# Kernel tuning notes

Hardware: AMD Instinct MI355X
Metric: run time of the kernel (lower is better)

## Reference

```python
import jax, jax.numpy as jnp
import numpy as np

NPG = 39      # nodes per graph, from (1+8+64+9)*(39+1)=3280 = lin1 in_features
NEG_SLOPE = 0.2


def gat_conv(x, src, dst, W, a_src, a_dst, b, n):
    """PyG GATConv, heads=1, self-loops already appended to (src, dst).
    x:[N,Fin] W:[Fin,Fout] a_src/a_dst:[Fout] b:[Fout] -> [N,Fout]"""
    h = x @ W                                        # [N,Fout]
    e = jax.nn.leaky_relu(h[src] @ a_src + h[dst] @ a_dst, NEG_SLOPE)  # [E]
    m = jax.lax.stop_gradient(jax.ops.segment_max(e, dst, num_segments=n))
    w = jnp.exp(e - m[dst])
    denom = jax.ops.segment_sum(w, dst, num_segments=n)
    alpha = w / (denom[dst] + 1e-16)                 # segment softmax per target node
    out = jax.ops.segment_sum(alpha[:, None] * h[src], dst, num_segments=n)
    return out + b


def setup_inputs() -> dict:
    key = jax.random.key(0)
    ks = jax.random.split(key, 20)
    B, DEG = 4096, 8
    N = B * NPG
    E = N * DEG
    x = jax.random.normal(ks[0], (N, 1), dtype=jnp.float32)
    # block-diagonal edges: each node emits DEG edges to random nodes in SAME graph
    src = jnp.repeat(jnp.arange(N, dtype=jnp.int64), DEG)
    offs = (src // NPG) * NPG
    dst = offs + jax.random.randint(ks[1], (E,), 0, NPG, dtype=jnp.int64)
    edge_index = jnp.stack([src, dst])
    batch_vec = jnp.repeat(jnp.arange(B, dtype=jnp.int64), NPG)

    def glorot(k, shape):
        fan = shape[0] + (shape[1] if len(shape) > 1 else 1)
        s = jnp.sqrt(6.0 / fan)
        return jax.random.uniform(k, shape, jnp.float32, -s, s)

    p = {
        'W1': glorot(ks[2], (1, 8)),   'a1s': glorot(ks[3], (8,)),  'a1d': glorot(ks[4], (8,)),  'b1': jnp.zeros((8,), jnp.float32),
        'W2': glorot(ks[5], (8, 64)),  'a2s': glorot(ks[6], (64,)), 'a2d': glorot(ks[7], (64,)), 'b2': jnp.zeros((64,), jnp.float32),
        'W3': glorot(ks[8], (64, 9)),  'a3s': glorot(ks[9], (9,)),  'a3d': glorot(ks[10], (9,)), 'b3': jnp.zeros((9,), jnp.float32),
        'lW1': glorot(ks[11], (3280, 5000)), 'lb1': jnp.zeros((5000,), jnp.float32),
        'lW2': glorot(ks[12], (5000, 1024)), 'lb2': jnp.zeros((1024,), jnp.float32),
        'lW3': glorot(ks[13], (1024, 9)),    'lb3': jnp.zeros((9,), jnp.float32),
    }
    return {'x': x, 'edge_index': edge_index, 'batch_vec': batch_vec, **p}


def reference(x, edge_index, batch_vec,
              W1, a1s, a1d, b1, W2, a2s, a2d, b2, W3, a3s, a3d, b3,
              lW1, lb1, lW2, lb2, lW3, lb3):
    N = x.shape[0]
    B = N // NPG
    loops = jnp.arange(N, dtype=edge_index.dtype)
    src = jnp.concatenate([edge_index[0], loops])   # GATConv add_self_loops=True
    dst = jnp.concatenate([edge_index[1], loops])

    res = x.reshape(B, -1)                                    # [B,39]
    out0 = jax.ops.segment_max(x, batch_vec, num_segments=B)  # [B,1]

    h1 = jax.nn.relu(gat_conv(x, src, dst, W1, a1s, a1d, b1, N))   # dropout = eval no-op
    res1 = h1.reshape(B, -1)                                   # [B,312]
    out1 = jax.ops.segment_max(h1, batch_vec, num_segments=B)

    h2 = jax.nn.relu(gat_conv(h1, src, dst, W2, a2s, a2d, b2, N))
    res2 = h2.reshape(B, -1)                                   # [B,2496]
    out2 = jax.ops.segment_max(h2, batch_vec, num_segments=B)

    h3 = jax.nn.relu(gat_conv(h2, src, dst, W3, a3s, a3d, b3, N))
    res3 = h3.reshape(B, -1)                                   # [B,351]
    out3 = jax.ops.segment_max(h3, batch_vec, num_segments=B)

    f = jnp.concatenate([res, res1, res2, res3, out0, out1, out2, out3], axis=1)  # [B,3280]
    f = jax.nn.relu(f @ lW1 + lb1)
    f = jax.nn.relu(f @ lW2 + lb2)
    return f @ lW3 + lb3                                       # [B,9]
```

## Files before the change

kernel.cpp:

```cpp
#include <hip/hip_runtime.h>
#include <hip/hip_bf16.h>
#include <hip/hip_fp16.h>
#include <stdint.h>


typedef float f32x4 __attribute__((ext_vector_type(4)));
typedef short bf16x8 __attribute__((ext_vector_type(8)));
typedef _Float16 f16x8 __attribute__((ext_vector_type(8)));

__device__ __forceinline__ unsigned fenc(float f) {
  int s = __float_as_int(f);
  return s < 0 ? ~(unsigned)s : ((unsigned)s | 0x80000000u);
}
__device__ __forceinline__ float fdec(unsigned u) {
  return (u & 0x80000000u) ? __int_as_float((int)(u & 0x7fffffffu))
                           : __int_as_float(~(int)u);
}

__device__ __forceinline__ void ldsbar() {
  asm volatile("s_waitcnt lgkmcnt(0)\n\ts_barrier" ::: "memory");
}


__global__ __launch_bounds__(128) void gnn_conv_seq(
    const float* __restrict__ x,
    const int* __restrict__ esrc, const int* __restrict__ edst,
    const float* __restrict__ W1, const float* __restrict__ a1s, const float* __restrict__ a1d, const float* __restrict__ b1,
    const float* __restrict__ W2, const float* __restrict__ a2s, const float* __restrict__ a2d, const float* __restrict__ b2,
    const float* __restrict__ W3, const float* __restrict__ a3s, const float* __restrict__ a3d, const float* __restrict__ b3,
    __hip_bfloat16* __restrict__ fA,
    const float* __restrict__ lW1, const float* __restrict__ lW2,
    short* __restrict__ W1T, short* __restrict__ W2T)
{
  __shared__ __align__(16) char smem[19200];
  const int tid = threadIdx.x;
  const int bid = blockIdx.x;

  if (bid >= 4096) {
    float (*t)[260] = (float(*)[260])smem;
    const int cid = bid - 4096;
    const float* W; short* WT; int ktile, ntile, K0, N0, KT;
    if (cid < 4160) { W = lW1; WT = W1T; ktile = cid % 208; ntile = cid / 208; K0 = 3280; N0 = 5000; KT = 52; }
    else { int c2 = cid - 4160; W = lW2; WT = W2T; ktile = c2 % 320; ntile = c2 / 320; K0 = 5000; N0 = 1024; KT = 80; }

    const int kb = ktile * 16, nb = ntile * 256;
    const int wv = tid >> 6, ln = tid & 63;
#pragma unroll
    for (int r = 0; r < 8; ++r) {
      int k = kb + wv * 8 + r;
      int n = nb + ln * 4;
      f32x4 v = (f32x4){0.f, 0.f, 0.f, 0.f};
      if (k < K0 && n < N0) v = *(const f32x4*)&W[(size_t)k * N0 + n];
      *(f32x4*)&t[wv * 8 + r][ln * 4] = v;
    }
    __syncthreads();
#pragma unroll
    for (int h = 0; h < 4; ++h) {
      int c = h * 128 + tid;
      int nl = c >> 1, kc = c & 1;
      int n = nb + nl, k = kb + kc * 8;
      union { bf16x8 v; __hip_bfloat16 b[8]; } z;
#pragma unroll
      for (int j = 0; j < 8; ++j) z.b[j] = __float2bfloat16(t[kc * 8 + j][nl]);
      int rt = n >> 7, mi = (n >> 4) & 7, lr = n & 15;
      int kt = k >> 6, kq = (k >> 5) & 1, lc = (k >> 3) & 3;
      size_t addr = ((((size_t)rt * KT) + kt) * 16 + mi * 2 + kq) * 512 + ((size_t)lr + 16 * lc) * 8;
      *(bf16x8*)&WT[addr] = z.v;
    }
    return;
  }

  float*    A     = (float*)   (smem);
  __half*   Hh2   = (__half*)  (smem + 6880);
  __half*   h1h   = (__half*)  (smem + 12512);
  float*    HfT   = (float*)   (smem + 13152);
  float*    sW3T  = (float*)   (smem + 14752);
  float*    xbuf  = (float*)   (smem + 17216);
  float*    a2buf = (float*)   (smem + 17376);
  float*    sarr  = (float*)   (smem + 17888);
  float*    darr  = (float*)   (smem + 18048);
  float*    den   = (float*)   (smem + 18208);
  unsigned* umax  = (unsigned*)(smem + 18368);
  unsigned* umx   = (unsigned*)(smem + 18528);
  float*    a3sb  = (float*)   (smem + 19056);
  float*    a3db  = (float*)   (smem + 19104);
  float*    b3b   = (float*)   (smem + 19152);

  const int g = bid, w = tid >> 6, f = tid & 63;

  const int rt = g >> 7, mi = (g >> 4) & 7, lrow = g & 15;
  const size_t gbase = (size_t)rt * 52 * 8192 + (size_t)(mi * 2) * 512 + (size_t)lrow * 8;
#define COLADDR(c) (gbase + (size_t)((c) >> 6) * 8192 + (size_t)(((c) >> 5) & 1) * 512 \
                    + (size_t)(((c) >> 3) & 3) * 128 + ((c) & 7))

  for (int i = tid; i < 576; i += 128) { int k = i / 9, f3 = i - 9 * k; sW3T[f3 * 68 + k] = W3[i]; }
  a2buf[tid] = (tid < 64) ? a2s[tid] : a2d[tid - 64];
  if (tid < 9) { a3sb[tid] = a3s[tid]; a3db[tid] = a3d[tid]; b3b[tid] = b3[tid]; }
  for (int i = tid; i < 132; i += 128) umx[i] = 0u;
  for (int i = tid; i < 430; i += 128) *(f32x4*)&A[i * 4] = (f32x4){0.f, 0.f, 0.f, 0.f};
  for (int i = tid; i < 400; i += 128) HfT[i] = 0.f;
  if (tid < 40) { den[tid] = 0.f; umax[tid] = 0u; xbuf[tid] = 0.f; }

  float xv = 0.f;
  if (tid < 39) { xv = x[g * 39 + tid]; xbuf[tid] = xv; fA[COLADDR(tid)] = __float2bfloat16(xv); }

  int els[3], eld[3];
  const int eb = g * 312, nb0 = g * 39;
#pragma unroll
  for (int it = 0; it < 3; ++it) {
    int e = it * 128 + tid, ls = -1, ld = 0;
    if (e < 351) {
      if (e < 312) { ls = esrc[eb + e] - nb0; ld = edst[eb + e] - nb0; }
      else         { ls = e - 312; ld = ls; }
    }
    els[it] = ls; eld[it] = ld;
  }
  float c_s = 0.f, c_d = 0.f;
  const float w1r = W1[tid & 7], b1r = b1[tid & 7];
#pragma unroll
  for (int ff = 0; ff < 8; ++ff) { float wv = W1[ff]; c_s += wv * a1s[ff]; c_d += wv * a1d[ff]; }
  ldsbar();

  if (tid < 39) atomicMax(&umx[0], fenc(xv));
  float ee[3];
#pragma unroll
  for (int it = 0; it < 3; ++it) {
    if (els[it] >= 0) {
      float e = xbuf[els[it]] * c_s + xbuf[eld[it]] * c_d;
      e = (e > 0.f) ? e : 0.2f * e;
      ee[it] = e;
      atomicMax(&umax[eld[it]], fenc(e));
    }
  }
  ldsbar();
#pragma unroll
  for (int it = 0; it < 3; ++it) {
    if (els[it] >= 0) {
      float wv = __expf(ee[it] - fdec(umax[eld[it]]));
      atomicAdd(&den[eld[it]], wv);
      atomicAdd(&A[eld[it] * 44 + els[it]], wv);
    }
  }
  ldsbar();
  if (tid < 39) {
    const float* Ar = &A[tid * 44];
    float q = 0.f;
#pragma unroll
    for (int c = 0; c < 10; ++c) {
      f32x4 a4 = *(const f32x4*)&Ar[c * 4];
      f32x4 x4 = *(const f32x4*)&xbuf[c * 4];
      q += a4.x * x4.x + a4.y * x4.y + a4.z * x4.z + a4.w * x4.w;
    }
    sarr[tid] = q * (1.f / (den[tid] + 1e-16f));
  }
  ldsbar();
#pragma unroll
  for (int it = 0; it < 3; ++it) {
    int slot = it * 128 + tid;
    if (slot < 312) {
      int i = slot >> 3, fi = slot & 7;
      float v = fmaxf(sarr[i] * w1r + b1r, 0.f);
      h1h[slot] = __float2half(v);
      fA[COLADDR(39 + slot)] = __float2bfloat16(v);
      atomicMax(&umx[1 + fi], fenc(v));
    }
  }
  ldsbar();

  float ht2r[40];
  {
    float w2k[8];
#pragma unroll
    for (int k = 0; k < 8; ++k) w2k[k] = W2[k * 64 + f];
#pragma unroll
    for (int i = 0; i < 39; ++i) {
      f16x8 hr = *(const f16x8*)&h1h[i * 8];
      float hv = 0.f;
#pragma unroll
      for (int k = 0; k < 8; ++k) hv += (float)hr[k] * w2k[k];
      ht2r[i] = hv;
    }
    ht2r[39] = 0.f;
#pragma unroll
    for (int i = 0; i < 39; ++i) {
      if ((i < 20) ? (w == 0) : (w == 1))
        Hh2[i * 72 + f] = __float2half(ht2r[i]);
    }
    for (int i = tid; i < 430; i += 128) *(f32x4*)&A[i * 4] = (f32x4){0.f, 0.f, 0.f, 0.f};
    if (tid < 39) { den[tid] = 0.f; umax[tid] = 0u; }
  }
  ldsbar();
  {
    int node = f;
    if (node < 39) {
      const float* ab = a2buf + (tid & 64);
      const __half* hr = &Hh2[node * 72];
      float s = 0.f;
#pragma unroll
      for (int c = 0; c < 8; ++c) {
        f16x8 hv = *(const f16x8*)&hr[c * 8];
        f32x4 a0 = *(const f32x4*)&ab[c * 8];
        f32x4 a1 = *(const f32x4*)&ab[c * 8 + 4];
        s += (float)hv[0] * a0.x + (float)hv[1] * a0.y + (float)hv[2] * a0.z + (float)hv[3] * a0.w
           + (float)hv[4] * a1.x + (float)hv[5] * a1.y + (float)hv[6] * a1.z + (float)hv[7] * a1.w;
      }
      if (tid < 64) sarr[node] = s; else darr[node] = s;
    }
  }
  ldsbar();
#pragma unroll
  for (int it = 0; it < 3; ++it) {
    if (els[it] >= 0) {
      float e = sarr[els[it]] + darr[eld[it]];
      e = (e > 0.f) ? e : 0.2f * e;
      ee[it] = e;
      atomicMax(&umax[eld[it]], fenc(e));
    }
  }
  ldsbar();
#pragma unroll
  for (int it = 0; it < 3; ++it) {
    if (els[it] >= 0) {
      float wv = __expf(ee[it] - fdec(umax[eld[it]]));
      atomicAdd(&den[eld[it]], wv);
      atomicAdd(&A[eld[it] * 44 + els[it]], wv);
    }
  }
  ldsbar();
  {
    const float b2r = b2[f];
    for (int it = 0; it < 20; ++it) {
      int i = it * 2 + w;
      if (i < 39) {
        float inv = 1.f / (den[i] + 1e-16f);
        const float* Ar = &A[i * 44];
        float acc = 0.f;
#pragma unroll
        for (int c = 0; c < 10; ++c) {
          f32x4 a4 = *(const f32x4*)&Ar[c * 4];
          acc += a4.x * ht2r[c * 4] + a4.y * ht2r[c * 4 + 1]
               + a4.z * ht2r[c * 4 + 2] + a4.w * ht2r[c * 4 + 3];
        }
        float v = fmaxf(acc * inv + b2r, 0.f);
        Hh2[i * 72 + f] = __float2half(v);
        fA[COLADDR(351 + i * 64 + f)] = __float2bfloat16(v);
        atomicMax(&umx[9 + f], fenc(v));
      }
    }
  }
  ldsbar();

  {
#pragma unroll
    for (int it = 0; it < 3; ++it) {
      int slot = it * 128 + tid;
      if (slot < 351) {
        int i = slot / 9, f3 = slot - 9 * i;
        const __half* hr = &Hh2[i * 72];
        const float* wr = &sW3T[f3 * 68];
        float acc = 0.f;
#pragma unroll
        for (int c = 0; c < 8; ++c) {
          f16x8 hv = *(const f16x8*)&hr[c * 8];
          f32x4 w0 = *(const f32x4*)&wr[c * 8];
          f32x4 w1 = *(const f32x4*)&wr[c * 8 + 4];
          acc += (float)hv[0] * w0.x + (float)hv[1] * w0.y + (float)hv[2] * w0.z + (float)hv[3] * w0.w
               + (float)hv[4] * w1.x + (float)hv[5] * w1.y + (float)hv[6] * w1.z + (float)hv[7] * w1.w;
        }
        HfT[f3 * 44 + i] = acc;
      }
    }
    for (int i = tid; i < 430; i += 128) *(f32x4*)&A[i * 4] = (f32x4){0.f, 0.f, 0.f, 0.f};
    if (tid < 39) { den[tid] = 0.f; umax[tid] = 0u; }
  }
  ldsbar();
  {
    int node = f;
    if (node < 39) {
      const float* av = (tid < 64) ? a3sb : a3db;
      float s = 0.f;
#pragma unroll
      for (int f3 = 0; f3 < 9; ++f3) s += HfT[f3 * 44 + node] * av[f3];
      if (tid < 64) sarr[node] = s; else darr[node] = s;
    }
  }
  ldsbar();
#pragma unroll
  for (int it = 0; it < 3; ++it) {
    if (els[it] >= 0) {
      float e = sarr[els[it]] + darr[eld[it]];
      e = (e > 0.f) ? e : 0.2f * e;
      ee[it] = e;
      atomicMax(&umax[eld[it]], fenc(e));
    }
  }
  ldsbar();
#pragma unroll
  for (int it = 0; it < 3; ++it) {
    if (els[it] >= 0) {
      float wv = __expf(ee[it] - fdec(umax[eld[it]]));
      atomicAdd(&den[eld[it]], wv);
      atomicAdd(&A[eld[it] * 44 + els[it]], wv);
    }
  }
  ldsbar();
#pragma unroll
  for (int it = 0; it < 3; ++it) {
    int slot = it * 128 + tid;
    if (slot < 351) {
      int i = slot / 9, f3 = slot - 9 * i;
      float inv = 1.f / (den[i] + 1e-16f);
      const float* Ar = &A[i * 44];
      const float* Hr = &HfT[f3 * 44];
      float acc = 0.f;
#pragma unroll
      for (int c = 0; c < 10; ++c) {
        f32x4 a4 = *(const f32x4*)&Ar[c * 4];
        f32x4 h4 = *(const f32x4*)&Hr[c * 4];
        acc += a4.x * h4.x + a4.y * h4.y + a4.z * h4.z + a4.w * h4.w;
      }
      float v = fmaxf(acc * inv + b3b[f3], 0.f);
      fA[COLADDR(2847 + slot)] = __float2bfloat16(v);
      atomicMax(&umx[73 + f3], fenc(v));
    }
  }
  ldsbar();

  if (tid < 130) {
    int c = 3198 + tid;
    float v = (tid < 82) ? fdec(umx[tid]) : 0.f;
    fA[COLADDR(c)] = __float2bfloat16(v);
  }
#undef COLADDR
}


__device__ __forceinline__ void gld_lds16(const void* gptr, void* l) {
  typedef const __attribute__((address_space(1))) unsigned int GU;
  typedef __attribute__((address_space(3))) unsigned int LU;
  __builtin_amdgcn_global_load_lds((GU*)gptr, (LU*)l, 16, 0, 0);
}

template<int MODE>
__global__ __launch_bounds__(256) void gemm_tiled(
    const short* __restrict__ A, const short* __restrict__ B,
    const float* __restrict__ bias, int Nreal,
    void* __restrict__ Cout, int Nn, int KT, int ktPerSplit, int outKT)
{
  __shared__ __align__(16) short lA[8192];
  __shared__ __align__(16) short lB[8192];
  const int tid = threadIdx.x;
  const int w = tid >> 6, L = tid & 63;
  const int lrow = L & 15, lch = L >> 4;
  const int mt = blockIdx.y, nt = blockIdx.x;
  const int mw = (w >> 1) * 4, nw = (w & 1) * 4;
  const int kt0 = blockIdx.z * ktPerSplit, kt1 = kt0 + ktPerSplit;

  const short* Ab = A + ((size_t)mt * KT) * 8192 + (size_t)L * 8;
  const short* Bb = B + ((size_t)nt * KT) * 8192 + (size_t)L * 8;

  f32x4 acc[4][4] = {};

  for (int kt = kt0; kt < kt1; ++kt) {
    const short* Ak = Ab + (size_t)kt * 8192;
    const short* Bk = Bb + (size_t)kt * 8192;
#pragma unroll
    for (int j = 0; j < 4; ++j) {
      int st = w * 4 + j;
      gld_lds16(Ak + st * 512, &lA[st * 512]);
      gld_lds16(Bk + st * 512, &lB[st * 512]);
    }
    __syncthreads();
#pragma unroll
    for (int kk = 0; kk < 2; ++kk) {
      bf16x8 af[4], bfr[4];
#pragma unroll
      for (int i = 0; i < 4; ++i) {
        af[i]  = *(const bf16x8*)&lA[((mw + i) * 2 + kk) * 512 + L * 8];
        bfr[i] = *(const bf16x8*)&lB[((nw + i) * 2 + kk) * 512 + L * 8];
      }
#pragma unroll
      for (int i = 0; i < 4; ++i)
#pragma unroll
        for (int j = 0; j < 4; ++j)
          acc[i][j] = __builtin_amdgcn_mfma_f32_16x16x32_bf16(af[i], bfr[j], acc[i][j], 0, 0, 0);
    }
    __syncthreads();
  }

  if (MODE == 0) {
    __hip_bfloat16* C = (__hip_bfloat16*)Cout;
#pragma unroll
    for (int j = 0; j < 4; ++j) {
      int n = nt * 128 + (nw + j) * 16 + lrow;
      float bn = (n < Nreal) ? bias[n] : 0.f;
      int kt = n >> 6, kq = (n >> 5) & 1, lc2 = (n >> 3) & 3, j2 = n & 7;
#pragma unroll
      for (int i = 0; i < 4; ++i) {
        int mi = mw + i;
        size_t base = ((((size_t)mt * outKT + kt) * 16) + mi * 2 + kq) * 512
                      + (size_t)(lch * 4) * 8 + (size_t)lc2 * 128 + j2;
#pragma unroll
        for (int r = 0; r < 4; ++r)
          C[base + r * 8] = __float2bfloat16(fmaxf(acc[i][j][r] + bn, 0.f));
      }
    }
  } else {
    __half* P = (__half*)Cout + (size_t)blockIdx.z * 4096 * 1024;
#pragma unroll
    for (int j = 0; j < 4; ++j) {
      int n = nt * 128 + (nw + j) * 16 + lrow;
#pragma unroll
      for (int i = 0; i < 4; ++i)
#pragma unroll
        for (int r = 0; r < 4; ++r) {
          int m = mt * 128 + (mw + i) * 16 + lch * 4 + r;
          P[(size_t)m * Nn + n] = __float2half(acc[i][j][r]);
        }
    }
  }
}


__global__ __launch_bounds__(256) void gemm3_fused(
    const __half* __restrict__ P,
    const float* __restrict__ b2v,
    const float* __restrict__ W3,
    const float* __restrict__ b3v,
    float* __restrict__ out)
{
  __shared__ float sW3[9 * 1024];
  int tid = threadIdx.x;
  for (int i = tid; i < 9216; i += 256) { int k = i / 9, j = i - 9 * k; sW3[j * 1024 + k] = W3[i]; }
  __syncthreads();
  int row = blockIdx.x * 4 + (tid >> 6);
  int lane = tid & 63;
  const __half* p0 = P + (size_t)row * 1024;
  const size_t S = (size_t)4096 * 1024;
  float acc[9] = {0, 0, 0, 0, 0, 0, 0, 0, 0};
  for (int t = 0; t < 16; ++t) {
    int k = lane + 64 * t;
    float c = __half2float(p0[k]) + __half2float(p0[k + S])
            + __half2float(p0[k + 2 * S]) + __half2float(p0[k + 3 * S]) + b2v[k];
    c = fmaxf(c, 0.f);
#pragma unroll
    for (int j = 0; j < 9; ++j) acc[j] += c * sW3[j * 1024 + k];
  }
#pragma unroll
  for (int j = 0; j < 9; ++j) {
    float v = acc[j];
    v += __shfl_down(v, 32, 64);
    v += __shfl_down(v, 16, 64);
    v += __shfl_down(v, 8, 64);
    v += __shfl_down(v, 4, 64);
    v += __shfl_down(v, 2, 64);
    v += __shfl_down(v, 1, 64);
    if (lane == 0) out[(size_t)row * 9 + j] = v + b3v[j];
  }
}


extern "C" void kernel_launch(void* const* d_in, const int* in_sizes, int n_in,
                              void* d_out, int out_size, void* d_ws, size_t ws_size,
                              hipStream_t stream)
{
  const float* x   = (const float*)d_in[0];
  const int*   ei  = (const int*)d_in[1];
  const float* W1  = (const float*)d_in[3];
  const float* a1s = (const float*)d_in[4];
  const float* a1d = (const float*)d_in[5];
  const float* b1  = (const float*)d_in[6];
  const float* W2  = (const float*)d_in[7];
  const float* a2s = (const float*)d_in[8];
  const float* a2d = (const float*)d_in[9];
  const float* b2  = (const float*)d_in[10];
  const float* W3  = (const float*)d_in[11];
  const float* a3s = (const float*)d_in[12];
  const float* a3d = (const float*)d_in[13];
  const float* b3  = (const float*)d_in[14];
  const float* lW1 = (const float*)d_in[15];
  const float* lb1 = (const float*)d_in[16];
  const float* lW2 = (const float*)d_in[17];
  const float* lb2 = (const float*)d_in[18];
  const float* lW3 = (const float*)d_in[19];
  const float* lb3 = (const float*)d_in[20];

  const int E = 4096 * 39 * 8;
  const int* esrc = ei;
  const int* edst = ei + E;

  short* fA  = (short*)d_ws;
  short* W1T = fA  + (size_t)4096 * 3328;
  short* C1  = W1T + (size_t)5120 * 3328;
  short* W2T = C1  + (size_t)4096 * 5120;
  __half* P  = (__half*)d_ws;

  gnn_conv_seq<<<9536, 128, 0, stream>>>(x, esrc, edst,
                                         W1, a1s, a1d, b1, W2, a2s, a2d, b2, W3, a3s, a3d, b3,
                                         (__hip_bfloat16*)fA, lW1, lW2, W1T, W2T);
  gemm_tiled<0><<<dim3(40, 32, 1), 256, 0, stream>>>(fA, W1T, lb1, 5000, C1, 5120, 52, 52, 80);
  gemm_tiled<1><<<dim3(8, 32, 4), 256, 0, stream>>>(C1, W2T, nullptr, 1024, P, 1024, 80, 20, 0);
  gemm3_fused<<<1024, 256, 0, stream>>>(P, lb2, lW3, lb3, (float*)d_out);
}
```

Baseline: 463.7 us.

## Replace per-edge atomic softmax with dense count-matrix attention per graph

Edges are counted once into a packed 4-bit multiplicity matrix (target x source) using a single atomic pass. Each GAT layer then computes attention densely over all 39x39 pairs, masked by the counts, with the max and sum found by thread-partial reductions rather than atomicMax/atomicAdd on shared memory. This removes per-layer atomics and the re-zeroing of the accumulation buffers, at the cost of evaluating about 1521 pairs instead of 351 edges and reusing scratch space in HfT/sW3T. A 4-bit count could overflow if more than 15 duplicate edges hit the same pair, which is very unlikely with these inputs.

```diff
diff --git a/kernel.cpp b/kernel.cpp
--- a/kernel.cpp
+++ b/kernel.cpp
@@ -32,7 +32,7 @@
     const float* __restrict__ lW1, const float* __restrict__ lW2,
     short* __restrict__ W1T, short* __restrict__ W2T)
 {
-  __shared__ __align__(16) char smem[19200];
+  __shared__ __align__(16) char smem[19840];
   const int tid = threadIdx.x;
   const int bid = blockIdx.x;
 
@@ -79,68 +79,91 @@
   float*    a2buf = (float*)   (smem + 17376);
   float*    sarr  = (float*)   (smem + 17888);
   float*    darr  = (float*)   (smem + 18048);
-  float*    den   = (float*)   (smem + 18208);
-  unsigned* umax  = (unsigned*)(smem + 18368);
-  unsigned* umx   = (unsigned*)(smem + 18528);
-  float*    a3sb  = (float*)   (smem + 19056);
-  float*    a3db  = (float*)   (smem + 19104);
-  float*    b3b   = (float*)   (smem + 19152);
+  unsigned* umx   = (unsigned*)(smem + 18208);
+  float*    a3sb  = (float*)   (smem + 18736);
+  float*    a3db  = (float*)   (smem + 18784);
+  float*    b3b   = (float*)   (smem + 18832);
+  unsigned* cntP  = (unsigned*)(smem + 18880);
 
   const int g = bid, w = tid >> 6, f = tid & 63;
+  const int dd3 = tid / 3, pp3 = tid - dd3 * 3;
 
   const int rt = g >> 7, mi = (g >> 4) & 7, lrow = g & 15;
   const size_t gbase = (size_t)rt * 52 * 8192 + (size_t)(mi * 2) * 512 + (size_t)lrow * 8;
 #define COLADDR(c) (gbase + (size_t)((c) >> 6) * 8192 + (size_t)(((c) >> 5) & 1) * 512 \
                     + (size_t)(((c) >> 3) & 3) * 128 + ((c) & 7))
 
+  auto denseE = [&](const float* sv, const float* dv, float* mxs) {
+    if (tid < 117) {
+      float dval = dv[dd3];
+      float mx = -1e30f;
+      float* Ar = &A[dd3 * 44];
+      int s0 = pp3 * 13;
+#pragma unroll
+      for (int k = 0; k < 13; ++k) {
+        int s = s0 + k;
+        float e = sv[s] + dval;
+        e = (e > 0.f) ? e : 0.2f * e;
+        Ar[s] = e;
+        unsigned c = (cntP[dd3 * 6 + (s >> 3)] >> (4 * (s & 7))) & 0xFu;
+        if (c) mx = fmaxf(mx, e);
+      }
+      mxs[tid] = mx;
+    }
+  };
+  auto denseW = [&](const float* mxs, float* sms) {
+    if (tid < 117) {
+      float m = fmaxf(fmaxf(mxs[dd3 * 3], mxs[dd3 * 3 + 1]), mxs[dd3 * 3 + 2]);
+      float* Ar = &A[dd3 * 44];
+      int s0 = pp3 * 13;
+      float sum = 0.f;
+#pragma unroll
+      for (int k = 0; k < 13; ++k) {
+        int s = s0 + k;
+        unsigned c = (cntP[dd3 * 6 + (s >> 3)] >> (4 * (s & 7))) & 0xFu;
+        float ex = __expf(Ar[s] - m);
+        float wv = c ? (float)c * ex : 0.f;
+        Ar[s] = wv; sum += wv;
+      }
+      if (pp3 == 2) Ar[39] = 0.f;
+      sms[tid] = sum;
+    }
+  };
+
   for (int i = tid; i < 576; i += 128) { int k = i / 9, f3 = i - 9 * k; sW3T[f3 * 68 + k] = W3[i]; }
   a2buf[tid] = (tid < 64) ? a2s[tid] : a2d[tid - 64];
   if (tid < 9) { a3sb[tid] = a3s[tid]; a3db[tid] = a3d[tid]; b3b[tid] = b3[tid]; }
   for (int i = tid; i < 132; i += 128) umx[i] = 0u;
-  for (int i = tid; i < 430; i += 128) *(f32x4*)&A[i * 4] = (f32x4){0.f, 0.f, 0.f, 0.f};
-  for (int i = tid; i < 400; i += 128) HfT[i] = 0.f;
-  if (tid < 40) { den[tid] = 0.f; umax[tid] = 0u; xbuf[tid] = 0.f; }
+  for (int i = tid; i < 234; i += 128) cntP[i] = 0u;
+  if (tid < 40) xbuf[tid] = 0.f;
 
   float xv = 0.f;
   if (tid < 39) { xv = x[g * 39 + tid]; xbuf[tid] = xv; fA[COLADDR(tid)] = __float2bfloat16(xv); }
 
-  int els[3], eld[3];
+  float c_s = 0.f, c_d = 0.f;
+  const float w1r = W1[tid & 7], b1r = b1[tid & 7];
+#pragma unroll
+  for (int ff = 0; ff < 8; ++ff) { float wv = W1[ff]; c_s += wv * a1s[ff]; c_d += wv * a1d[ff]; }
   const int eb = g * 312, nb0 = g * 39;
+  ldsbar();
+
+  if (tid < 39) atomicMax(&umx[0], fenc(xv));
 #pragma unroll
   for (int it = 0; it < 3; ++it) {
-    int e = it * 128 + tid, ls = -1, ld = 0;
+    int e = it * 128 + tid;
     if (e < 351) {
+      int ls, ld;
       if (e < 312) { ls = esrc[eb + e] - nb0; ld = edst[eb + e] - nb0; }
       else         { ls = e - 312; ld = ls; }
-    }
-    els[it] = ls; eld[it] = ld;
-  }
-  float c_s = 0.f, c_d = 0.f;
-  const float w1r = W1[tid & 7], b1r = b1[tid & 7];
-#pragma unroll
-  for (int ff = 0; ff < 8; ++ff) { float wv = W1[ff]; c_s += wv * a1s[ff]; c_d += wv * a1d[ff]; }
-  ldsbar();
-
-  if (tid < 39) atomicMax(&umx[0], fenc(xv));
-  float ee[3];
-#pragma unroll
-  for (int it = 0; it < 3; ++it) {
-    if (els[it] >= 0) {
-      float e = xbuf[els[it]] * c_s + xbuf[eld[it]] * c_d;
-      e = (e > 0.f) ? e : 0.2f * e;
-      ee[it] = e;
-      atomicMax(&umax[eld[it]], fenc(e));
-    }
-  }
-  ldsbar();
-#pragma unroll
-  for (int it = 0; it < 3; ++it) {
-    if (els[it] >= 0) {
-      float wv = __expf(ee[it] - fdec(umax[eld[it]]));
-      atomicAdd(&den[eld[it]], wv);
-      atomicAdd(&A[eld[it] * 44 + els[it]], wv);
-    }
-  }
+      atomicAdd(&cntP[ld * 6 + (ls >> 3)], 1u << (4 * (ls & 7)));
+    }
+  }
+  if (f < 39) { if (w == 0) sarr[f] = xbuf[f] * c_s; else darr[f] = xbuf[f] * c_d; }
+  ldsbar();
+
+  denseE(sarr, darr, &HfT[0]);
+  ldsbar();
+  denseW(&HfT[0], &HfT[128]);
   ldsbar();
   if (tid < 39) {
     const float* Ar = &A[tid * 44];
@@ -151,7 +174,8 @@
       f32x4 x4 = *(const f32x4*)&xbuf[c * 4];
       q += a4.x * x4.x + a4.y * x4.y + a4.z * x4.z + a4.w * x4.w;
     }
-    sarr[tid] = q * (1.f / (den[tid] + 1e-16f));
+    float inv = 1.f / (HfT[128 + 3 * tid] + HfT[129 + 3 * tid] + HfT[130 + 3 * tid] + 1e-16f);
+    sarr[tid] = q * inv;
   }
   ldsbar();
 #pragma unroll
@@ -186,8 +210,6 @@
       if ((i < 20) ? (w == 0) : (w == 1))
         Hh2[i * 72 + f] = __float2half(ht2r[i]);
     }
-    for (int i = tid; i < 430; i += 128) *(f32x4*)&A[i * 4] = (f32x4){0.f, 0.f, 0.f, 0.f};
-    if (tid < 39) { den[tid] = 0.f; umax[tid] = 0u; }
   }
   ldsbar();
   {
@@ -208,31 +230,16 @@
     }
   }
   ldsbar();
-#pragma unroll
-  for (int it = 0; it < 3; ++it) {
-    if (els[it] >= 0) {
-      float e = sarr[els[it]] + darr[eld[it]];
-      e = (e > 0.f) ? e : 0.2f * e;
-      ee[it] = e;
-      atomicMax(&umax[eld[it]], fenc(e));
-    }
-  }
-  ldsbar();
-#pragma unroll
-  for (int it = 0; it < 3; ++it) {
-    if (els[it] >= 0) {
-      float wv = __expf(ee[it] - fdec(umax[eld[it]]));
-      atomicAdd(&den[eld[it]], wv);
-      atomicAdd(&A[eld[it] * 44 + els[it]], wv);
-    }
-  }
+  denseE(sarr, darr, &HfT[0]);
+  ldsbar();
+  denseW(&HfT[0], &HfT[128]);
   ldsbar();
   {
     const float b2r = b2[f];
     for (int it = 0; it < 20; ++it) {
       int i = it * 2 + w;
       if (i < 39) {
-        float inv = 1.f / (den[i] + 1e-16f);
+        float inv = 1.f / (HfT[128 + 3 * i] + HfT[129 + 3 * i] + HfT[130 + 3 * i] + 1e-16f);
         const float* Ar = &A[i * 44];
         float acc = 0.f;
 #pragma unroll
@@ -270,8 +277,7 @@
         HfT[f3 * 44 + i] = acc;
       }
     }
-    for (int i = tid; i < 430; i += 128) *(f32x4*)&A[i * 4] = (f32x4){0.f, 0.f, 0.f, 0.f};
-    if (tid < 39) { den[tid] = 0.f; umax[tid] = 0u; }
+    if (tid < 9) HfT[tid * 44 + 39] = 0.f;
   }
   ldsbar();
   {
@@ -285,31 +291,16 @@
     }
   }
   ldsbar();
-#pragma unroll
-  for (int it = 0; it < 3; ++it) {
-    if (els[it] >= 0) {
-      float e = sarr[els[it]] + darr[eld[it]];
-      e = (e > 0.f) ? e : 0.2f * e;
-      ee[it] = e;
-      atomicMax(&umax[eld[it]], fenc(e));
-    }
-  }
-  ldsbar();
-#pragma unroll
-  for (int it = 0; it < 3; ++it) {
-    if (els[it] >= 0) {
-      float wv = __expf(ee[it] - fdec(umax[eld[it]]));
-      atomicAdd(&den[eld[it]], wv);
-      atomicAdd(&A[eld[it] * 44 + els[it]], wv);
-    }
-  }
+  denseE(sarr, darr, &sW3T[0]);
+  ldsbar();
+  denseW(&sW3T[0], &sW3T[128]);
   ldsbar();
 #pragma unroll
   for (int it = 0; it < 3; ++it) {
     int slot = it * 128 + tid;
     if (slot < 351) {
       int i = slot / 9, f3 = slot - 9 * i;
-      float inv = 1.f / (den[i] + 1e-16f);
+      float inv = 1.f / (sW3T[128 + 3 * i] + sW3T[129 + 3 * i] + sW3T[130 + 3 * i] + 1e-16f);
       const float* Ar = &A[i * 44];
       const float* Hr = &HfT[f3 * 44];
       float acc = 0.f;
```

Measured after the change: 452.3 us. 2.5% less time.
